# Optimization experiments

Measured on AMD Instinct MI355X. Metric: run time of the kernel, lower is better.

Reference implementation:

```python
import jax, jax.numpy as jnp
import numpy as np

B, N, L, D, H = 2, 2048, 2048, 1024, 16
HD = D // H  # 64


def setup_inputs() -> dict:
    key = jax.random.key(0)
    ks = jax.random.split(key, 12)
    s = 0.02
    return {
        "x_q": jax.random.normal(ks[0], (B, N, D), jnp.float32),
        "x_kv": jax.random.normal(ks[1], (B, L, D), jnp.float32),
        "pad_mask": jax.random.randint(ks[2], (B, L), 0, 2) > 0,
        "wq": jax.random.normal(ks[3], (D, D), jnp.float32) * s,
        "bq": jnp.zeros((D,), jnp.float32),
        "wk": jax.random.normal(ks[4], (D, D), jnp.float32) * s,
        "bk": jnp.zeros((D,), jnp.float32),
        "wv": jax.random.normal(ks[5], (D, D), jnp.float32) * s,
        "bv": jnp.zeros((D,), jnp.float32),
        "wo": jax.random.normal(ks[6], (D, D), jnp.float32) * s,
        "bo": jnp.zeros((D,), jnp.float32),
    }


def reference(x_q, x_kv, pad_mask, wq, bq, wk, bk, wv, bv, wo, bo):
    scale = HD ** -0.5
    # projections: (B, S, D) -> (B, H, S, HD)
    def split_heads(x):
        return x.reshape(x.shape[0], x.shape[1], H, HD).transpose(0, 2, 1, 3)
    q = split_heads(x_q @ wq + bq) * scale
    k = split_heads(x_kv @ wk + bk)
    v = split_heads(x_kv @ wv + bv)
    attn = jnp.einsum('bhic,bhjc->bhij', q, k)  # (B, H, N, L)
    neg = -jnp.finfo(attn.dtype).max
    attn = jnp.where(pad_mask[:, None, None, :], neg, attn)
    attn = jax.nn.softmax(attn, axis=-1)
    o = jnp.einsum('bhij,bhjc->bhic', attn, v)  # (B, H, N, HD)
    o = o.transpose(0, 2, 1, 3).reshape(B, N, D)
    return o @ wo + bo
```

## Files before the change

### kernel.cpp

```cpp
#include <hip/hip_runtime.h>
#include <hip/hip_bf16.h>
#include <math.h>

typedef __bf16 bf16;
typedef __attribute__((ext_vector_type(8))) __bf16 bf16x8;
typedef __attribute__((ext_vector_type(4))) __bf16 bf16x4;
typedef __attribute__((ext_vector_type(4))) float floatx4;

#define BB 2
#define NN 2048
#define LL 2048
#define DD 1024
#define HH 16
#define HDD 64

#define QSCALE (0.125f * 1.44269504f)
#define PCLAMP 21.66f
#define MBIAS  (-100000.0f)

__device__ __forceinline__ void async16(const bf16* g, bf16* l) {
  __builtin_amdgcn_global_load_lds((const __attribute__((address_space(1))) void*)(g),
                                   (__attribute__((address_space(3))) void*)(l), 16, 0, 0);
}

__global__ void detect_mask_kernel(const unsigned* __restrict__ m, int* __restrict__ flag) {
  __shared__ int hasBig, hasFloat;
  if (threadIdx.x == 0) { hasBig = 0; hasFloat = 0; }
  __syncthreads();
  int big = 0, flt = 0;
  for (int idx = threadIdx.x; idx < 1024; idx += 256) {
    unsigned v = m[idx];
    if (v == 0x3F800000u) flt = 1;
    else if (v > 1u) big = 1;
  }
  if (big) atomicOr(&hasBig, 1);
  if (flt) atomicOr(&hasFloat, 1);
  __syncthreads();
  if (threadIdx.x == 0) *flag = hasFloat ? 2 : (hasBig ? 1 : 0);
}

__global__ __launch_bounds__(256) void convert_kernel(
    const float* __restrict__ src, bf16* __restrict__ dst, int n)
{
  int idx = (blockIdx.x * 256 + threadIdx.x) * 8;
  if (idx >= n) return;
  floatx4 a = *(const floatx4*)&src[idx];
  floatx4 b = *(const floatx4*)&src[idx + 4];
  bf16x8 o;
#pragma unroll
  for (int e = 0; e < 4; e++) { o[e] = (bf16)a[e]; o[4 + e] = (bf16)b[e]; }
  *(bf16x8*)&dst[idx] = o;
}

__global__ __launch_bounds__(256) void wtrans_kernel(
    const float* __restrict__ W0, const float* __restrict__ W1,
    const float* __restrict__ W2, const float* __restrict__ W3,
    bf16* __restrict__ T0, bf16* __restrict__ T1,
    bf16* __restrict__ T2, bf16* __restrict__ T3)
{
  __shared__ bf16 Tb[64][72];
  const int bid = blockIdx.x;
  const int which = bid >> 8;
  const float* W = which == 0 ? W0 : which == 1 ? W1 : which == 2 ? W2 : W3;
  bf16*       T = which == 0 ? T0 : which == 1 ? T1 : which == 2 ? T2 : T3;
  const int tile = bid & 255;
  const int k0 = (tile >> 4) * 64, n0 = (tile & 15) * 64;
  const int t = threadIdx.x;
  const int r = t >> 2;
  const int c = (t & 3) * 16;
  const float* Wr = W + (size_t)(k0 + r) * 1024 + n0 + c;
  floatx4 f0 = *(const floatx4*)(Wr + 0);
  floatx4 f1 = *(const floatx4*)(Wr + 4);
  floatx4 f2 = *(const floatx4*)(Wr + 8);
  floatx4 f3 = *(const floatx4*)(Wr + 12);
#pragma unroll
  for (int e = 0; e < 4; e++) {
    Tb[c + e][r]      = (bf16)f0[e];
    Tb[c + 4 + e][r]  = (bf16)f1[e];
    Tb[c + 8 + e][r]  = (bf16)f2[e];
    Tb[c + 12 + e][r] = (bf16)f3[e];
  }
  __syncthreads();
  bf16* Tr = T + (size_t)(n0 + r) * 1024 + k0 + c;
  *(bf16x8*)&Tr[0] = *(const bf16x8*)&Tb[r][c];
  *(bf16x8*)&Tr[8] = *(const bf16x8*)&Tb[r][c + 8];
}

template <typename TC>
__device__ __forceinline__ void gemm_body(
    int bx, const bf16* __restrict__ A, const bf16* __restrict__ Wt,
    const float* __restrict__ bias, TC* __restrict__ C, float scale, int transv)
{
  __shared__ bf16 As[128 * 64];
  __shared__ bf16 Bs[64 * 64];

  const int tm = bx >> 4, tn = bx & 15;
  const int m0 = tm * 128, n0 = tn * 64;
  const int t = threadIdx.x;
  const int w = t >> 6, l = t & 63;
  const int q = l >> 4, i = l & 15;
  const int wm = (w >> 1) * 64, wn = (w & 1) * 32;
  const int sr = t >> 3;
  const int sc = (t & 7) * 8;

  const floatx4 zero = {0.f, 0.f, 0.f, 0.f};
  floatx4 acc[4][2];
#pragma unroll
  for (int mi = 0; mi < 4; mi++)
#pragma unroll
    for (int ni = 0; ni < 2; ni++) acc[mi][ni] = zero;

  for (int k0 = 0; k0 < 1024; k0 += 64) {
    __syncthreads();
#pragma unroll
    for (int j = 0; j < 4; j++)
      async16(&A[(size_t)(m0 + j * 32 + sr) * 1024 + k0 + sc], &As[(j * 32 + sr) * 64 + sc]);
#pragma unroll
    for (int j = 0; j < 2; j++)
      async16(&Wt[(size_t)(n0 + j * 32 + sr) * 1024 + k0 + sc], &Bs[(j * 32 + sr) * 64 + sc]);
    __syncthreads();
#pragma unroll
    for (int ks = 0; ks < 2; ks++) {
      bf16x8 af[4], bfr[2];
#pragma unroll
      for (int mi = 0; mi < 4; mi++)
        af[mi] = *(const bf16x8*)&As[(wm + mi * 16 + i) * 64 + ks * 32 + q * 8];
#pragma unroll
      for (int ni = 0; ni < 2; ni++)
        bfr[ni] = *(const bf16x8*)&Bs[(wn + ni * 16 + i) * 64 + ks * 32 + q * 8];
#pragma unroll
      for (int mi = 0; mi < 4; mi++)
#pragma unroll
        for (int ni = 0; ni < 2; ni++)
          acc[mi][ni] = __builtin_amdgcn_mfma_f32_16x16x32_bf16(af[mi], bfr[ni], acc[mi][ni], 0, 0, 0);
    }
  }
#pragma unroll
  for (int ni = 0; ni < 2; ni++) {
    int col = n0 + wn + ni * 16 + i;
    float bv = bias[col];
#pragma unroll
    for (int mi = 0; mi < 4; mi++) {
      int row = m0 + wm + mi * 16 + q * 4;
      if (transv) {
        int bb = row >> 11, key = row & 2047;
        bf16x4 v4;
#pragma unroll
        for (int r = 0; r < 4; r++) v4[r] = (bf16)(acc[mi][ni][r] + bv);
        *(bf16x4*)&((bf16*)C)[(size_t)bb * (DD * (size_t)LL) + (size_t)col * LL + key] = v4;
      } else {
#pragma unroll
        for (int r = 0; r < 4; r++)
          C[(size_t)(row + r) * 1024 + col] = (TC)((acc[mi][ni][r] + bv) * scale);
      }
    }
  }
}

__global__ __launch_bounds__(256) void qkv_gemm(
    const bf16* __restrict__ Xq, const bf16* __restrict__ Xkv,
    const bf16* __restrict__ Wtq, const bf16* __restrict__ Wtk, const bf16* __restrict__ Wtv,
    const float* __restrict__ bq, const float* __restrict__ bk, const float* __restrict__ bv,
    bf16* __restrict__ Qp, bf16* __restrict__ Kp, bf16* __restrict__ VtG, int shift)
{
  const int bid = blockIdx.x;
  const int which = bid >> shift;
  const int bx = bid & ((1 << shift) - 1);
  if (which == 0)      gemm_body<bf16>(bx, Xq,  Wtq, bq, Qp,  QSCALE, 0);
  else if (which == 1) gemm_body<bf16>(bx, Xkv, Wtk, bk, Kp,  1.0f,   0);
  else                 gemm_body<bf16>(bx, Xkv, Wtv, bv, VtG, 1.0f,   1);
}

__global__ __launch_bounds__(256) void out_gemm(
    const bf16* __restrict__ A, const bf16* __restrict__ Wt,
    const float* __restrict__ bias, float* __restrict__ C)
{
  gemm_body<float>(blockIdx.x, A, Wt, bias, C, 1.0f, 0);
}

__global__ __launch_bounds__(256) void attn_kernel(
    const bf16* __restrict__ Q, const bf16* __restrict__ K,
    const bf16* __restrict__ Vt, const void* __restrict__ mask,
    const int* __restrict__ flag, bf16* __restrict__ O, int mbase)
{
  __shared__ bf16 Ks[64][72];
  __shared__ bf16 Vs[64][72];
  __shared__ bf16 Ps[4][16][72];
  __shared__ float biasL[2048];

  const int bid = blockIdx.x;
  const int qt = bid & 31;
  const int h  = (bid >> 5) & 15;
  const int b  = bid >> 9;
  const int t = threadIdx.x;
  const int w = t >> 6, lane = t & 63;
  const int q = lane >> 4, i = lane & 15;

  const int mode = *flag;
  const int mb = mbase + b;
  {
    const int base = t * 8;
    if (mode == 0) {
      const int* mm = ((const int*)mask) + mb * LL + base;
#pragma unroll
      for (int e = 0; e < 8; e++) biasL[base + e] = mm[e] ? MBIAS : 0.0f;
    } else if (mode == 1) {
      const unsigned char* mm = ((const unsigned char*)mask) + mb * LL + base;
#pragma unroll
      for (int e = 0; e < 8; e++) biasL[base + e] = mm[e] ? MBIAS : 0.0f;
    } else {
      const float* mm = ((const float*)mask) + mb * LL + base;
#pragma unroll
      for (int e = 0; e < 8; e++) biasL[base + e] = (mm[e] != 0.0f) ? MBIAS : 0.0f;
    }
  }

  const bf16* Qb = Q  + (size_t)b * (NN * DD) + h * HDD;
  const bf16* Kb = K  + (size_t)b * (LL * DD) + h * HDD;
  const bf16* Vb = Vt + (size_t)b * (DD * (size_t)LL) + (size_t)(h * HDD) * LL;

  const int qrow = qt * 64 + w * 16;
  bf16x8 qfrag[2];
#pragma unroll
  for (int ks = 0; ks < 2; ks++)
    qfrag[ks] = *(const bf16x8*)&Qb[(size_t)(qrow + i) * DD + ks * 32 + q * 8];

  const floatx4 zero = {0.f, 0.f, 0.f, 0.f};
  floatx4 oacc[4];
#pragma unroll
  for (int n = 0; n < 4; n++) oacc[n] = zero;
  float psum = 0.0f;

  const int ldr = t >> 3;
  const int ldc = (t & 7) * 8;

  for (int kt = 0; kt < LL; kt += 64) {
    __syncthreads();
    *(bf16x8*)&Ks[ldr][ldc]      = *(const bf16x8*)&Kb[(size_t)(kt + ldr) * DD + ldc];
    *(bf16x8*)&Ks[ldr + 32][ldc] = *(const bf16x8*)&Kb[(size_t)(kt + ldr + 32) * DD + ldc];
    *(bf16x8*)&Vs[ldr][ldc]      = *(const bf16x8*)&Vb[(size_t)ldr * LL + kt + ldc];
    *(bf16x8*)&Vs[ldr + 32][ldc] = *(const bf16x8*)&Vb[(size_t)(ldr + 32) * LL + kt + ldc];
    __syncthreads();

#pragma unroll
    for (int n = 0; n < 4; n++) {
      floatx4 bv = *(const floatx4*)&biasL[kt + n * 16 + q * 4];
      floatx4 a = bv;
#pragma unroll
      for (int ks = 0; ks < 2; ks++) {
        bf16x8 kf = *(const bf16x8*)&Ks[n * 16 + i][ks * 32 + q * 8];
        a = __builtin_amdgcn_mfma_f32_16x16x32_bf16(kf, qfrag[ks], a, 0, 0, 0);
      }
      bf16x4 v4;
#pragma unroll
      for (int r = 0; r < 4; r++) {
        float p = __builtin_amdgcn_exp2f(fminf(a[r], PCLAMP));
        psum += p;
        v4[r] = (bf16)p;
      }
      *(bf16x4*)&Ps[w][i][n * 16 + q * 4] = v4;
    }
    bf16x8 pf[2];
#pragma unroll
    for (int ks = 0; ks < 2; ks++)
      pf[ks] = *(const bf16x8*)&Ps[w][i][ks * 32 + q * 8];
#pragma unroll
    for (int n = 0; n < 4; n++) {
#pragma unroll
      for (int ks = 0; ks < 2; ks++) {
        bf16x8 vf = *(const bf16x8*)&Vs[n * 16 + i][ks * 32 + q * 8];
        oacc[n] = __builtin_amdgcn_mfma_f32_16x16x32_bf16(vf, pf[ks], oacc[n], 0, 0, 0);
      }
    }
  }

  psum += __shfl_xor(psum, 16, 64);
  psum += __shfl_xor(psum, 32, 64);
  float inv = 1.0f / fmaxf(psum, 1e-30f);

  bf16* Ob = O + (size_t)b * (NN * DD) + h * HDD;
#pragma unroll
  for (int n = 0; n < 4; n++) {
    bf16x4 v4;
#pragma unroll
    for (int r = 0; r < 4; r++) v4[r] = (bf16)(oacc[n][r] * inv);
    *(bf16x4*)&Ob[(size_t)(qrow + i) * DD + n * 16 + q * 4] = v4;
  }
}

extern "C" void kernel_launch(void* const* d_in, const int* in_sizes, int n_in,
                              void* d_out, int out_size, void* d_ws, size_t ws_size,
                              hipStream_t stream)
{
  const float* x_q  = (const float*)d_in[0];
  const float* x_kv = (const float*)d_in[1];
  const void*  pad  = d_in[2];
  const float* wq = (const float*)d_in[3];
  const float* bq = (const float*)d_in[4];
  const float* wk = (const float*)d_in[5];
  const float* bk = (const float*)d_in[6];
  const float* wv = (const float*)d_in[7];
  const float* bv = (const float*)d_in[8];
  const float* wo = (const float*)d_in[9];
  const float* bo = (const float*)d_in[10];
  float* out = (float*)d_out;

  char* ws = (char*)d_ws;
  const size_t MB = (size_t)1 << 20;
  const size_t fullElems = (size_t)BB * NN * DD;
  const size_t batchElems = (size_t)NN * DD;

  int* flag = (int*)((char*)d_out + (size_t)out_size * sizeof(float) - 16);
  detect_mask_kernel<<<1, 256, 0, stream>>>((const unsigned*)pad, flag);

  if (ws_size >= 48 * MB) {
    bf16* Xqb  = (bf16*)(ws);
    bf16* Xkvb = (bf16*)(ws + 8 * MB);
    bf16* Wtq  = (bf16*)(ws + 16 * MB);
    bf16* Wtk  = (bf16*)(ws + 18 * MB);
    bf16* Wtv  = (bf16*)(ws + 20 * MB);
    bf16* Wto  = (bf16*)(ws + 22 * MB);
    bf16* Qp   = (bf16*)(ws + 24 * MB);
    bf16* Kp   = (bf16*)(ws + 32 * MB);
    bf16* VtG  = (bf16*)(ws + 40 * MB);
    bf16* Op   = Xqb;

    convert_kernel<<<2048, 256, 0, stream>>>(x_q,  Xqb,  (int)fullElems);
    convert_kernel<<<2048, 256, 0, stream>>>(x_kv, Xkvb, (int)fullElems);
    wtrans_kernel<<<1024, 256, 0, stream>>>(wq, wk, wv, wo, Wtq, Wtk, Wtv, Wto);
    qkv_gemm<<<1536, 256, 0, stream>>>(Xqb, Xkvb, Wtq, Wtk, Wtv, bq, bk, bv, Qp, Kp, VtG, 9);
    attn_kernel<<<1024, 256, 0, stream>>>(Qp, Kp, VtG, pad, flag, Op, 0);
    out_gemm<<<512, 256, 0, stream>>>(Op, Wto, bo, out);
  } else {
    bf16* Wtq  = (bf16*)(ws);
    bf16* Wtk  = (bf16*)(ws + 2 * MB);
    bf16* Wtv  = (bf16*)(ws + 4 * MB);
    bf16* Wto  = (bf16*)(ws + 6 * MB);
    bf16* Xqb  = (bf16*)(ws + 8 * MB);
    bf16* Xkvb = (bf16*)(ws + 12 * MB);
    bf16* Qp   = (bf16*)(ws + 16 * MB);
    bf16* Kp   = (bf16*)(ws + 20 * MB);
    bf16* VtG  = (bf16*)(ws + 24 * MB);
    bf16* Op   = Xqb;

    wtrans_kernel<<<1024, 256, 0, stream>>>(wq, wk, wv, wo, Wtq, Wtk, Wtv, Wto);
    for (int b = 0; b < BB; b++) {
      convert_kernel<<<1024, 256, 0, stream>>>(x_q  + b * batchElems, Xqb,  (int)batchElems);
      convert_kernel<<<1024, 256, 0, stream>>>(x_kv + b * batchElems, Xkvb, (int)batchElems);
      qkv_gemm<<<768, 256, 0, stream>>>(Xqb, Xkvb, Wtq, Wtk, Wtv, bq, bk, bv, Qp, Kp, VtG, 8);
      attn_kernel<<<512, 256, 0, stream>>>(Qp, Kp, VtG, pad, flag, Op, b);
      out_gemm<<<256, 256, 0, stream>>>(Op, Wto, bo, out + b * batchElems);
    }
  }
}
```

Measured before the change: 248.2 us.

## Enlarge GEMM tiles to 128x128 and attention query tiles to 128 rows

The GEMM tile grows from 128x64 to 128x128, giving each wave a 64x64 sub-tile with 16 accumulators so A fragments are reused across more MFMAs. The attention kernel now handles 32 query rows per wave (128 per block), so each K/V tile loaded into shared memory serves twice as many queries and the fragment reads are shared by two MFMA groups. Grid sizes are halved to match. The trade-off is higher register and LDS use and fewer blocks: 512 attention blocks and 256 output GEMM blocks on a 256-CU part, which may reduce occupancy and latency hiding.

Result: slower. 271.5 us (+9.4%).

```diff
diff --git a/kernel.cpp b/kernel.cpp
--- a/kernel.cpp
+++ b/kernel.cpp
@@ -92,23 +92,23 @@
     const float* __restrict__ bias, TC* __restrict__ C, float scale, int transv)
 {
   __shared__ bf16 As[128 * 64];
-  __shared__ bf16 Bs[64 * 64];
-
-  const int tm = bx >> 4, tn = bx & 15;
-  const int m0 = tm * 128, n0 = tn * 64;
+  __shared__ bf16 Bs[128 * 64];
+
+  const int tm = bx >> 3, tn = bx & 7;
+  const int m0 = tm * 128, n0 = tn * 128;
   const int t = threadIdx.x;
   const int w = t >> 6, l = t & 63;
   const int q = l >> 4, i = l & 15;
-  const int wm = (w >> 1) * 64, wn = (w & 1) * 32;
+  const int wm = (w >> 1) * 64, wn = (w & 1) * 64;
   const int sr = t >> 3;
   const int sc = (t & 7) * 8;
 
   const floatx4 zero = {0.f, 0.f, 0.f, 0.f};
-  floatx4 acc[4][2];
+  floatx4 acc[4][4];
 #pragma unroll
   for (int mi = 0; mi < 4; mi++)
 #pragma unroll
-    for (int ni = 0; ni < 2; ni++) acc[mi][ni] = zero;
+    for (int ni = 0; ni < 4; ni++) acc[mi][ni] = zero;
 
   for (int k0 = 0; k0 < 1024; k0 += 64) {
     __syncthreads();
@@ -116,27 +116,27 @@
     for (int j = 0; j < 4; j++)
       async16(&A[(size_t)(m0 + j * 32 + sr) * 1024 + k0 + sc], &As[(j * 32 + sr) * 64 + sc]);
 #pragma unroll
-    for (int j = 0; j < 2; j++)
+    for (int j = 0; j < 4; j++)
       async16(&Wt[(size_t)(n0 + j * 32 + sr) * 1024 + k0 + sc], &Bs[(j * 32 + sr) * 64 + sc]);
     __syncthreads();
 #pragma unroll
     for (int ks = 0; ks < 2; ks++) {
-      bf16x8 af[4], bfr[2];
+      bf16x8 af[4], bfr[4];
 #pragma unroll
       for (int mi = 0; mi < 4; mi++)
         af[mi] = *(const bf16x8*)&As[(wm + mi * 16 + i) * 64 + ks * 32 + q * 8];
 #pragma unroll
-      for (int ni = 0; ni < 2; ni++)
+      for (int ni = 0; ni < 4; ni++)
         bfr[ni] = *(const bf16x8*)&Bs[(wn + ni * 16 + i) * 64 + ks * 32 + q * 8];
 #pragma unroll
       for (int mi = 0; mi < 4; mi++)
 #pragma unroll
-        for (int ni = 0; ni < 2; ni++)
+        for (int ni = 0; ni < 4; ni++)
           acc[mi][ni] = __builtin_amdgcn_mfma_f32_16x16x32_bf16(af[mi], bfr[ni], acc[mi][ni], 0, 0, 0);
     }
   }
 #pragma unroll
-  for (int ni = 0; ni < 2; ni++) {
+  for (int ni = 0; ni < 4; ni++) {
     int col = n0 + wn + ni * 16 + i;
     float bv = bias[col];
 #pragma unroll
@@ -185,13 +185,13 @@
 {
   __shared__ bf16 Ks[64][72];
   __shared__ bf16 Vs[64][72];
-  __shared__ bf16 Ps[4][16][72];
+  __shared__ bf16 Ps[4][32][72];
   __shared__ float biasL[2048];
 
   const int bid = blockIdx.x;
-  const int qt = bid & 31;
-  const int h  = (bid >> 5) & 15;
-  const int b  = bid >> 9;
+  const int qt = bid & 15;
+  const int h  = (bid >> 4) & 15;
+  const int b  = bid >> 8;
   const int t = threadIdx.x;
   const int w = t >> 6, lane = t & 63;
   const int q = lane >> 4, i = lane & 15;
@@ -219,17 +219,21 @@
   const bf16* Kb = K  + (size_t)b * (LL * DD) + h * HDD;
   const bf16* Vb = Vt + (size_t)b * (DD * (size_t)LL) + (size_t)(h * HDD) * LL;
 
-  const int qrow = qt * 64 + w * 16;
-  bf16x8 qfrag[2];
-#pragma unroll
-  for (int ks = 0; ks < 2; ks++)
-    qfrag[ks] = *(const bf16x8*)&Qb[(size_t)(qrow + i) * DD + ks * 32 + q * 8];
+  const int qrow = qt * 128 + w * 32;
+  bf16x8 qfrag[2][2];
+#pragma unroll
+  for (int g = 0; g < 2; g++)
+#pragma unroll
+    for (int ks = 0; ks < 2; ks++)
+      qfrag[g][ks] = *(const bf16x8*)&Qb[(size_t)(qrow + g * 16 + i) * DD + ks * 32 + q * 8];
 
   const floatx4 zero = {0.f, 0.f, 0.f, 0.f};
-  floatx4 oacc[4];
-#pragma unroll
-  for (int n = 0; n < 4; n++) oacc[n] = zero;
-  float psum = 0.0f;
+  floatx4 oacc[2][4];
+#pragma unroll
+  for (int g = 0; g < 2; g++)
+#pragma unroll
+    for (int n = 0; n < 4; n++) oacc[g][n] = zero;
+  float psum[2] = {0.f, 0.f};
 
   const int ldr = t >> 3;
   const int ldc = (t & 7) * 8;
@@ -244,47 +248,56 @@
 
 #pragma unroll
     for (int n = 0; n < 4; n++) {
+      bf16x8 kf0 = *(const bf16x8*)&Ks[n * 16 + i][q * 8];
+      bf16x8 kf1 = *(const bf16x8*)&Ks[n * 16 + i][32 + q * 8];
       floatx4 bv = *(const floatx4*)&biasL[kt + n * 16 + q * 4];
-      floatx4 a = bv;
-#pragma unroll
-      for (int ks = 0; ks < 2; ks++) {
-        bf16x8 kf = *(const bf16x8*)&Ks[n * 16 + i][ks * 32 + q * 8];
-        a = __builtin_amdgcn_mfma_f32_16x16x32_bf16(kf, qfrag[ks], a, 0, 0, 0);
+#pragma unroll
+      for (int g = 0; g < 2; g++) {
+        floatx4 a = __builtin_amdgcn_mfma_f32_16x16x32_bf16(kf0, qfrag[g][0], bv, 0, 0, 0);
+        a = __builtin_amdgcn_mfma_f32_16x16x32_bf16(kf1, qfrag[g][1], a, 0, 0, 0);
+        bf16x4 v4;
+#pragma unroll
+        for (int r = 0; r < 4; r++) {
+          float p = __builtin_amdgcn_exp2f(fminf(a[r], PCLAMP));
+          psum[g] += p;
+          v4[r] = (bf16)p;
+        }
+        *(bf16x4*)&Ps[w][g * 16 + i][n * 16 + q * 4] = v4;
       }
+    }
+    bf16x8 pf[2][2];
+#pragma unroll
+    for (int g = 0; g < 2; g++)
+#pragma unroll
+      for (int ks = 0; ks < 2; ks++)
+        pf[g][ks] = *(const bf16x8*)&Ps[w][g * 16 + i][ks * 32 + q * 8];
+#pragma unroll
+    for (int n = 0; n < 4; n++) {
+      bf16x8 vf0 = *(const bf16x8*)&Vs[n * 16 + i][q * 8];
+      bf16x8 vf1 = *(const bf16x8*)&Vs[n * 16 + i][32 + q * 8];
+#pragma unroll
+      for (int g = 0; g < 2; g++) {
+        oacc[g][n] = __builtin_amdgcn_mfma_f32_16x16x32_bf16(vf0, pf[g][0], oacc[g][n], 0, 0, 0);
+        oacc[g][n] = __builtin_amdgcn_mfma_f32_16x16x32_bf16(vf1, pf[g][1], oacc[g][n], 0, 0, 0);
+      }
+    }
+  }
+
+  bf16* Ob = O + (size_t)b * (NN * DD) + h * HDD;
+#pragma unroll
+  for (int g = 0; g < 2; g++) {
+    float ps = psum[g];
+    ps += __shfl_xor(ps, 16, 64);
+    ps += __shfl_xor(ps, 32, 64);
+    float inv = 1.0f / fmaxf(ps, 1e-30f);
+    const size_t rbase = (size_t)(qrow + g * 16 + i) * DD;
+#pragma unroll
+    for (int n = 0; n < 4; n++) {
       bf16x4 v4;
 #pragma unroll
-      for (int r = 0; r < 4; r++) {
-        float p = __builtin_amdgcn_exp2f(fminf(a[r], PCLAMP));
-        psum += p;
-        v4[r] = (bf16)p;
-      }
-      *(bf16x4*)&Ps[w][i][n * 16 + q * 4] = v4;
-    }
-    bf16x8 pf[2];
-#pragma unroll
-    for (int ks = 0; ks < 2; ks++)
-      pf[ks] = *(const bf16x8*)&Ps[w][i][ks * 32 + q * 8];
-#pragma unroll
-    for (int n = 0; n < 4; n++) {
-#pragma unroll
-      for (int ks = 0; ks < 2; ks++) {
-        bf16x8 vf = *(const bf16x8*)&Vs[n * 16 + i][ks * 32 + q * 8];
-        oacc[n] = __builtin_amdgcn_mfma_f32_16x16x32_bf16(vf, pf[ks], oacc[n], 0, 0, 0);
-      }
-    }
-  }
-
-  psum += __shfl_xor(psum, 16, 64);
-  psum += __shfl_xor(psum, 32, 64);
-  float inv = 1.0f / fmaxf(psum, 1e-30f);
-
-  bf16* Ob = O + (size_t)b * (NN * DD) + h * HDD;
-#pragma unroll
-  for (int n = 0; n < 4; n++) {
-    bf16x4 v4;
-#pragma unroll
-    for (int r = 0; r < 4; r++) v4[r] = (bf16)(oacc[n][r] * inv);
-    *(bf16x4*)&Ob[(size_t)(qrow + i) * DD + n * 16 + q * 4] = v4;
+      for (int r = 0; r < 4; r++) v4[r] = (bf16)(oacc[g][n][r] * inv);
+      *(bf16x4*)&Ob[rbase + n * 16 + q * 4] = v4;
+    }
   }
 }
 
@@ -328,9 +341,9 @@
     convert_kernel<<<2048, 256, 0, stream>>>(x_q,  Xqb,  (int)fullElems);
     convert_kernel<<<2048, 256, 0, stream>>>(x_kv, Xkvb, (int)fullElems);
     wtrans_kernel<<<1024, 256, 0, stream>>>(wq, wk, wv, wo, Wtq, Wtk, Wtv, Wto);
-    qkv_gemm<<<1536, 256, 0, stream>>>(Xqb, Xkvb, Wtq, Wtk, Wtv, bq, bk, bv, Qp, Kp, VtG, 9);
-    attn_kernel<<<1024, 256, 0, stream>>>(Qp, Kp, VtG, pad, flag, Op, 0);
-    out_gemm<<<512, 256, 0, stream>>>(Op, Wto, bo, out);
+    qkv_gemm<<<768, 256, 0, stream>>>(Xqb, Xkvb, Wtq, Wtk, Wtv, bq, bk, bv, Qp, Kp, VtG, 8);
+    attn_kernel<<<512, 256, 0, stream>>>(Qp, Kp, VtG, pad, flag, Op, 0);
+    out_gemm<<<256, 256, 0, stream>>>(Op, Wto, bo, out);
   } else {
     bf16* Wtq  = (bf16*)(ws);
     bf16* Wtk  = (bf16*)(ws + 2 * MB);
@@ -347,9 +360,9 @@
     for (int b = 0; b < BB; b++) {
       convert_kernel<<<1024, 256, 0, stream>>>(x_q  + b * batchElems, Xqb,  (int)batchElems);
       convert_kernel<<<1024, 256, 0, stream>>>(x_kv + b * batchElems, Xkvb, (int)batchElems);
-      qkv_gemm<<<768, 256, 0, stream>>>(Xqb, Xkvb, Wtq, Wtk, Wtv, bq, bk, bv, Qp, Kp, VtG, 8);
-      attn_kernel<<<512, 256, 0, stream>>>(Qp, Kp, VtG, pad, flag, Op, b);
-      out_gemm<<<256, 256, 0, stream>>>(Op, Wto, bo, out + b * batchElems);
-    }
-  }
-}
+      qkv_gemm<<<384, 256, 0, stream>>>(Xqb, Xkvb, Wtq, Wtk, Wtv, bq, bk, bv, Qp, Kp, VtG, 7);
+      attn_kernel<<<256, 256, 0, stream>>>(Qp, Kp, VtG, pad, flag, Op, b);
+      out_gemm<<<128, 256, 0, stream>>>(Op, Wto, bo, out + b * batchElems);
+    }
+  }
+}
```

## Prefetch K/V tiles into registers, remap attention blocks, merge convert launches

Applied to the files above, without the earlier changes.

The attention loop now loads the next K/V tile into registers while the current tile is being computed, which hides global-load latency behind the MFMA work. Block indices are reordered so that consecutive blocks share a query tile across heads and batches rather than walking one head's query tiles in turn, which changes L2 locality. The two fp32-to-bf16 conversion launches are merged into one kernel to save a launch. In exchange, register pressure rises and one redundant wrap-around tile is loaded on the last iteration.

Measured after the change: 244.1 us. About the same (-1.7%).

```diff
diff --git a/kernel.cpp b/kernel.cpp
--- a/kernel.cpp
+++ b/kernel.cpp
@@ -39,17 +39,21 @@
   if (threadIdx.x == 0) *flag = hasFloat ? 2 : (hasBig ? 1 : 0);
 }
 
-__global__ __launch_bounds__(256) void convert_kernel(
-    const float* __restrict__ src, bf16* __restrict__ dst, int n)
-{
-  int idx = (blockIdx.x * 256 + threadIdx.x) * 8;
+__global__ __launch_bounds__(256) void convert2_kernel(
+    const float* __restrict__ srcA, bf16* __restrict__ dstA,
+    const float* __restrict__ srcB, bf16* __restrict__ dstB, int nb, int n)
+{
+  int gid = blockIdx.x;
+  const float* s = srcA; bf16* d = dstA;
+  if (gid >= nb) { s = srcB; d = dstB; gid -= nb; }
+  int idx = (gid * 256 + threadIdx.x) * 8;
   if (idx >= n) return;
-  floatx4 a = *(const floatx4*)&src[idx];
-  floatx4 b = *(const floatx4*)&src[idx + 4];
+  floatx4 a = *(const floatx4*)&s[idx];
+  floatx4 b = *(const floatx4*)&s[idx + 4];
   bf16x8 o;
 #pragma unroll
   for (int e = 0; e < 4; e++) { o[e] = (bf16)a[e]; o[4 + e] = (bf16)b[e]; }
-  *(bf16x8*)&dst[idx] = o;
+  *(bf16x8*)&d[idx] = o;
 }
 
 __global__ __launch_bounds__(256) void wtrans_kernel(
@@ -181,7 +185,7 @@
 __global__ __launch_bounds__(256) void attn_kernel(
     const bf16* __restrict__ Q, const bf16* __restrict__ K,
     const bf16* __restrict__ Vt, const void* __restrict__ mask,
-    const int* __restrict__ flag, bf16* __restrict__ O, int mbase)
+    const int* __restrict__ flag, bf16* __restrict__ O, int hbits, int mbase)
 {
   __shared__ bf16 Ks[64][72];
   __shared__ bf16 Vs[64][72];
@@ -189,9 +193,10 @@
   __shared__ float biasL[2048];
 
   const int bid = blockIdx.x;
-  const int qt = bid & 31;
-  const int h  = (bid >> 5) & 15;
-  const int b  = bid >> 9;
+  const int qt = bid >> hbits;
+  const int hb = bid & ((1 << hbits) - 1);
+  const int h  = (hbits == 5) ? (hb >> 1) : hb;
+  const int b  = (hbits == 5) ? (hb & 1) : 0;
   const int t = threadIdx.x;
   const int w = t >> 6, lane = t & 63;
   const int q = lane >> 4, i = lane & 15;
@@ -234,13 +239,26 @@
   const int ldr = t >> 3;
   const int ldc = (t & 7) * 8;
 
+  bf16x8 pk0 = *(const bf16x8*)&Kb[(size_t)ldr * DD + ldc];
+  bf16x8 pk1 = *(const bf16x8*)&Kb[(size_t)(ldr + 32) * DD + ldc];
+  bf16x8 pv0 = *(const bf16x8*)&Vb[(size_t)ldr * LL + ldc];
+  bf16x8 pv1 = *(const bf16x8*)&Vb[(size_t)(ldr + 32) * LL + ldc];
+
   for (int kt = 0; kt < LL; kt += 64) {
     __syncthreads();
-    *(bf16x8*)&Ks[ldr][ldc]      = *(const bf16x8*)&Kb[(size_t)(kt + ldr) * DD + ldc];
-    *(bf16x8*)&Ks[ldr + 32][ldc] = *(const bf16x8*)&Kb[(size_t)(kt + ldr + 32) * DD + ldc];
-    *(bf16x8*)&Vs[ldr][ldc]      = *(const bf16x8*)&Vb[(size_t)ldr * LL + kt + ldc];
-    *(bf16x8*)&Vs[ldr + 32][ldc] = *(const bf16x8*)&Vb[(size_t)(ldr + 32) * LL + kt + ldc];
+    *(bf16x8*)&Ks[ldr][ldc]      = pk0;
+    *(bf16x8*)&Ks[ldr + 32][ldc] = pk1;
+    *(bf16x8*)&Vs[ldr][ldc]      = pv0;
+    *(bf16x8*)&Vs[ldr + 32][ldc] = pv1;
     __syncthreads();
+
+    {
+      const int ktn = (kt + 64) & (LL - 1);
+      pk0 = *(const bf16x8*)&Kb[(size_t)(ktn + ldr) * DD + ldc];
+      pk1 = *(const bf16x8*)&Kb[(size_t)(ktn + ldr + 32) * DD + ldc];
+      pv0 = *(const bf16x8*)&Vb[(size_t)ldr * LL + ktn + ldc];
+      pv1 = *(const bf16x8*)&Vb[(size_t)(ldr + 32) * LL + ktn + ldc];
+    }
 
 #pragma unroll
     for (int n = 0; n < 4; n++) {
@@ -325,11 +343,10 @@
     bf16* VtG  = (bf16*)(ws + 40 * MB);
     bf16* Op   = Xqb;
 
-    convert_kernel<<<2048, 256, 0, stream>>>(x_q,  Xqb,  (int)fullElems);
-    convert_kernel<<<2048, 256, 0, stream>>>(x_kv, Xkvb, (int)fullElems);
+    convert2_kernel<<<4096, 256, 0, stream>>>(x_q, Xqb, x_kv, Xkvb, 2048, (int)fullElems);
     wtrans_kernel<<<1024, 256, 0, stream>>>(wq, wk, wv, wo, Wtq, Wtk, Wtv, Wto);
     qkv_gemm<<<1536, 256, 0, stream>>>(Xqb, Xkvb, Wtq, Wtk, Wtv, bq, bk, bv, Qp, Kp, VtG, 9);
-    attn_kernel<<<1024, 256, 0, stream>>>(Qp, Kp, VtG, pad, flag, Op, 0);
+    attn_kernel<<<1024, 256, 0, stream>>>(Qp, Kp, VtG, pad, flag, Op, 5, 0);
     out_gemm<<<512, 256, 0, stream>>>(Op, Wto, bo, out);
   } else {
     bf16* Wtq  = (bf16*)(ws);
@@ -345,10 +362,11 @@
 
     wtrans_kernel<<<1024, 256, 0, stream>>>(wq, wk, wv, wo, Wtq, Wtk, Wtv, Wto);
     for (int b = 0; b < BB; b++) {
-      convert_kernel<<<1024, 256, 0, stream>>>(x_q  + b * batchElems, Xqb,  (int)batchElems);
-      convert_kernel<<<1024, 256, 0, stream>>>(x_kv + b * batchElems, Xkvb, (int)batchElems);
+      convert2_kernel<<<2048, 256, 0, stream>>>(x_q + b * batchElems, Xqb,
+                                                x_kv + b * batchElems, Xkvb,
+                                                1024, (int)batchElems);
       qkv_gemm<<<768, 256, 0, stream>>>(Xqb, Xkvb, Wtq, Wtk, Wtv, bq, bk, bv, Qp, Kp, VtG, 8);
-      attn_kernel<<<512, 256, 0, stream>>>(Qp, Kp, VtG, pad, flag, Op, b);
+      attn_kernel<<<512, 256, 0, stream>>>(Qp, Kp, VtG, pad, flag, Op, 4, b);
       out_gemm<<<256, 256, 0, stream>>>(Op, Wto, bo, out + b * batchElems);
     }
   }
```
